# Kernel tuning notes

Measured on AMD Instinct MI355X. Metric: run time of the kernel, lower is better.

The kernel has to match this reference:

```python
import jax, jax.numpy as jnp
import numpy as np

B, S, I, H, L, A = 32768, 1, 128, 256, 2, 32


def setup_inputs() -> dict:
    key = jax.random.key(0)
    ks = jax.random.split(key, 16)
    s_in = 1.0 / np.sqrt(H)  # PyTorch GRU init scale
    def u(k, shape):
        return jax.random.uniform(k, shape, jnp.float32, -s_in, s_in)
    return {
        "x": jax.random.normal(ks[0], (B, S, I), jnp.float32),
        "h": jax.random.normal(ks[1], (L, B, H), jnp.float32),
        # layer 0 GRU params (gate order: r, z, n as in PyTorch)
        "w_ih0": u(ks[2], (3 * H, I)),
        "w_hh0": u(ks[3], (3 * H, H)),
        "b_ih0": u(ks[4], (3 * H,)),
        "b_hh0": u(ks[5], (3 * H,)),
        # layer 1 GRU params
        "w_ih1": u(ks[6], (3 * H, H)),
        "w_hh1": u(ks[7], (3 * H, H)),
        "b_ih1": u(ks[8], (3 * H,)),
        "b_hh1": u(ks[9], (3 * H,)),
        # heads
        "w_p": u(ks[10], (A, H)),
        "b_p": u(ks[11], (A,)),
        "w_v": u(ks[12], (1, H)),
        "b_v": u(ks[13], (1,)),
    }


def _gru_cell(x, h, w_ih, w_hh, b_ih, b_hh):
    # x: [B, in], h: [B, H]; PyTorch GRUCell math with gate order r,z,n
    gi = x @ w_ih.T + b_ih          # [B, 3H]
    gh = h @ w_hh.T + b_hh          # [B, 3H]
    i_r, i_z, i_n = jnp.split(gi, 3, axis=-1)
    h_r, h_z, h_n = jnp.split(gh, 3, axis=-1)
    r = jax.nn.sigmoid(i_r + h_r)
    z = jax.nn.sigmoid(i_z + h_z)
    n = jnp.tanh(i_n + r * h_n)
    return (1.0 - z) * n + z * h


def reference(x, h, w_ih0, w_hh0, b_ih0, b_hh0, w_ih1, w_hh1, b_ih1, b_hh1,
              w_p, b_p, w_v, b_v):
    xt = x[:, -1, :]  # seq len 1 -> single step
    h0 = _gru_cell(xt, h[0], w_ih0, w_hh0, b_ih0, b_hh0)
    h1 = _gru_cell(h0, h[1], w_ih1, w_hh1, b_ih1, b_hh1)
    logits = h1 @ w_p.T + b_p                 # [B, A]
    value = (h1 @ w_v.T + b_v)[:, 0]          # [B]
    h_new = jnp.stack([h0, h1], axis=0)       # [L, B, H]
    return logits, value, h_new
```

## Files before the change

### kernel.cpp

```cpp
#include <hip/hip_runtime.h>
#include <hip/hip_bf16.h>
#include <stdint.h>

#define NB 32768
#define ID 128
#define HD 256
#define AD 32
#define BM 32
#define MT 2
#define NTH 256
#define NBLK (NB / BM)

typedef unsigned int u32;
typedef unsigned short u16;
typedef __attribute__((ext_vector_type(8))) short bf16x8;
typedef __attribute__((ext_vector_type(4))) float f32x4;
typedef __attribute__((ext_vector_type(2))) u32 u32x2;

#define OFF_W0X 0
#define OFF_W0H 98304
#define OFF_W1X 294912
#define OFF_W1H 491520
#define OFF_WHD 688128
#define W_TOTAL 700416

__device__ __forceinline__ u16 f2bf(float f) {
    u32 u = __builtin_bit_cast(u32, f);
    return (u16)((u + 0x7FFFu + ((u >> 16) & 1u)) >> 16);
}
__device__ __forceinline__ float bf2f(u16 b) {
    return __builtin_bit_cast(float, (u32)b << 16);
}
__device__ __forceinline__ float sigf(float v) { return 1.0f / (1.0f + __expf(-v)); }
__device__ __forceinline__ float tanh_fast(float v) { return 1.0f - 2.0f / (1.0f + __expf(2.0f * v)); }

__global__ void prep_weights(const float* __restrict__ wih0, const float* __restrict__ whh0,
                             const float* __restrict__ wih1, const float* __restrict__ whh1,
                             const float* __restrict__ wp, const float* __restrict__ wv,
                             u16* __restrict__ wb) {
    int i = blockIdx.x * blockDim.x + threadIdx.x;
    if (i >= W_TOTAL) return;
    float v;
    if (i < OFF_W0H)      v = wih0[i];
    else if (i < OFF_W1X) v = whh0[i - OFF_W0H];
    else if (i < OFF_W1H) v = wih1[i - OFF_W1X];
    else if (i < OFF_WHD) v = whh1[i - OFF_W1H];
    else {
        int j = i - OFF_WHD;
        int r = j >> 8, k = j & 255;
        v = (r < AD) ? wp[j] : ((r == AD) ? wv[k] : 0.0f);
    }
    wb[i] = f2bf(v);
}

#define SWZ(row, kbyte, rowstride) ((((row) * (rowstride)) + (kbyte)) ^ (((row) & 7) << 4))

#define MFMA(a, b, c) __builtin_amdgcn_mfma_f32_16x16x32_bf16((a), (b), (c), 0, 0, 0)

template<int KXS>
__device__ __forceinline__ void stage_step(char* dst, const u16* __restrict__ Wx,
                                           const u16* __restrict__ Wh,
                                           int s, int cbase, int w, int lane) {
    const bool xside = s < KXS;
    const u16* W = xside ? Wx : Wh;
    const int KW = xside ? KXS * 32 : HD;
    const int ks = xside ? s : s - KXS;
#pragma unroll
    for (int i = 0; i < 3; ++i) {
        const int unit = w * 3 + i;
        const int ldsrow = unit * 16 + (lane >> 2);
        const int slot = lane & 3;
        const int g = ldsrow >> 6, colr = ldsrow & 63;
        const int kslot = slot ^ ((ldsrow >> 1) & 3);
        const u16* src = W + (size_t)(g * HD + cbase + colr) * KW + ks * 32 + kslot * 8;
        __builtin_amdgcn_global_load_lds(
            (const __attribute__((address_space(1))) void*)src,
            (__attribute__((address_space(3))) void*)(dst + unit * 1024),
            16, 0, 0);
    }
}

__device__ __forceinline__ bf16x8 read_wfrag(const char* buf, int g, int colw, int kg) {
    const int row = g * 64 + colw;
    const int slot = kg ^ ((row >> 1) & 3);
    return *(const bf16x8*)(buf + row * 64 + slot * 16);
}

template<int KXS>
__device__ __forceinline__ void gru_layer_v3(
    const char* __restrict__ Ax, const char* __restrict__ Ah,
    char* __restrict__ wb0, char* __restrict__ wb1,
    const u16* __restrict__ Wx, const u16* __restrict__ Wh,
    const float* __restrict__ bi, const float* __restrict__ bh,
    int lane, int w, u32 st[4][MT][2])
{
    constexpr int NS = KXS + 8;
    const int arow = lane & 15;
    const int kg = lane >> 4;
    const int colw = (w << 4) + arow;

#pragma unroll 1
    for (int c = 0; c < 4; ++c) {
        const int cbase = c * 64;
        const int col = cbase + colw;
        const float br  = bi[col] + bh[col];
        const float bz  = bi[HD + col] + bh[HD + col];
        const float bni = bi[2 * HD + col];
        const float bnh = bh[2 * HD + col];
        f32x4 accr[MT], accz[MT], accni[MT], accnh[MT];
#pragma unroll
        for (int m = 0; m < MT; ++m) {
            accr[m]  = f32x4{br, br, br, br};
            accz[m]  = f32x4{bz, bz, bz, bz};
            accni[m] = f32x4{bni, bni, bni, bni};
            accnh[m] = f32x4{bnh, bnh, bnh, bnh};
        }

        stage_step<KXS>(wb0, Wx, Wh, 0, cbase, w, lane);
        __syncthreads();

#pragma unroll
        for (int s = 0; s < NS; ++s) {
            char* cur = (s & 1) ? wb1 : wb0;
            char* nxt = (s & 1) ? wb0 : wb1;
            if (s + 1 < NS)
                stage_step<KXS>(nxt, Wx, Wh, s + 1, cbase, w, lane);
            bf16x8 w0 = read_wfrag(cur, 0, colw, kg);
            bf16x8 w1 = read_wfrag(cur, 1, colw, kg);
            bf16x8 w2 = read_wfrag(cur, 2, colw, kg);
            const bool xside = (s < KXS);
            const int kb2 = ((xside ? s : s - KXS) * 32 + kg * 8) * 2;
#pragma unroll
            for (int m = 0; m < MT; ++m) {
                const int row = m * 16 + arow;
                bf16x8 a = xside ? *(const bf16x8*)(Ax + SWZ(row, kb2, KXS * 64))
                                 : *(const bf16x8*)(Ah + SWZ(row, kb2, 512));
                accr[m] = MFMA(a, w0, accr[m]);
                accz[m] = MFMA(a, w1, accz[m]);
                if (xside) accni[m] = MFMA(a, w2, accni[m]);
                else       accnh[m] = MFMA(a, w2, accnh[m]);
            }
            __syncthreads();
        }

#pragma unroll
        for (int m = 0; m < MT; ++m) {
            const int rowg = m * 16 + ((lane >> 4) << 2);
#pragma unroll
            for (int pq = 0; pq < 2; ++pq) {
                u32 pk = 0;
#pragma unroll
                for (int q2 = 0; q2 < 2; ++q2) {
                    const int q = pq * 2 + q2;
                    float rg = sigf(accr[m][q]);
                    float zg = sigf(accz[m][q]);
                    float n  = tanh_fast(accni[m][q] + rg * accnh[m][q]);
                    float hp = bf2f(*(const u16*)(Ah + SWZ(rowg + q, col * 2, 512)));
                    float hv = (1.0f - zg) * n + zg * hp;
                    pk |= (u32)f2bf(hv) << (16 * q2);
                }
                st[c][m][pq] = pk;
            }
        }
    }
}

__device__ __forceinline__ void write_stash(char* __restrict__ R, u32 st[4][MT][2],
                                            int lane, int w) {
#pragma unroll
    for (int c = 0; c < 4; ++c)
#pragma unroll
        for (int m = 0; m < MT; ++m) {
            const int colb = (c * 64 + (w << 4) + (lane & 15)) * 2;
            const int rowg = m * 16 + ((lane >> 4) << 2);
            *(u16*)(R + SWZ(rowg + 0, colb, 512)) = (u16)(st[c][m][0]);
            *(u16*)(R + SWZ(rowg + 1, colb, 512)) = (u16)(st[c][m][0] >> 16);
            *(u16*)(R + SWZ(rowg + 2, colb, 512)) = (u16)(st[c][m][1]);
            *(u16*)(R + SWZ(rowg + 3, colb, 512)) = (u16)(st[c][m][1] >> 16);
        }
}

__device__ __forceinline__ void dump_h(const char* __restrict__ R,
                                       float* __restrict__ g, int row0, int t) {
#pragma unroll
    for (int it = 0; it < 8; ++it) {
        int i = t + it * NTH;
        int row = i >> 6, f4 = i & 63;
        u32x2 b = *(const u32x2*)(R + SWZ(row, f4 * 8, 512));
        f32x4 v;
        v[0] = __builtin_bit_cast(float, (b[0] & 0xFFFFu) << 16);
        v[1] = __builtin_bit_cast(float, b[0] & 0xFFFF0000u);
        v[2] = __builtin_bit_cast(float, (b[1] & 0xFFFFu) << 16);
        v[3] = __builtin_bit_cast(float, b[1] & 0xFFFF0000u);
        __builtin_nontemporal_store(v, (f32x4*)(g + (size_t)(row0 + row) * HD + f4 * 4));
    }
}

__global__ __launch_bounds__(NTH, 2) void gru_mfma(
    const float* __restrict__ x, const float* __restrict__ h,
    const float* __restrict__ bih0, const float* __restrict__ bhh0,
    const float* __restrict__ bih1, const float* __restrict__ bhh1,
    const float* __restrict__ bp, const float* __restrict__ bv,
    const u16* __restrict__ wb, float* __restrict__ out)
{
    __shared__ uint4 lds4[65536 / 16];
    char* lds = (char*)lds4;
    char* R1 = lds;
    char* R2 = lds + 8192;
    char* R3 = lds + 24576;
    char* WB0 = lds + 40960;
    char* WB1 = lds + 53248;

    const int t = threadIdx.x;
    const int lane = t & 63;
    const int w = t >> 6;
    const int row0 = blockIdx.x * BM;

    const u16* W0x = wb + OFF_W0X;
    const u16* W0h = wb + OFF_W0H;
    const u16* W1x = wb + OFF_W1X;
    const u16* W1h = wb + OFF_W1H;
    const u16* Whd = wb + OFF_WHD;

    float* out_logits = out;
    float* out_value  = out + (size_t)NB * AD;
    float* out_h0     = out_value + NB;
    float* out_h1     = out_h0 + (size_t)NB * HD;

    {
        const f32x4* xg = (const f32x4*)(x + (size_t)row0 * ID);
#pragma unroll
        for (int it = 0; it < 4; ++it) {
            int i = t + it * NTH;
            f32x4 v = __builtin_nontemporal_load(xg + i);
            int rowi = i >> 5;
            int kb = (i & 31) * 8;
            u32x2 b;
            b[0] = (u32)f2bf(v[0]) | ((u32)f2bf(v[1]) << 16);
            b[1] = (u32)f2bf(v[2]) | ((u32)f2bf(v[3]) << 16);
            *(u32x2*)(R1 + SWZ(rowi, kb, 256)) = b;
        }
        const f32x4* h0g = (const f32x4*)(h + (size_t)row0 * HD);
        const f32x4* h1g = (const f32x4*)(h + (size_t)NB * HD + (size_t)row0 * HD);
#pragma unroll
        for (int it = 0; it < 8; ++it) {
            int i = t + it * NTH;
            int rowi = i >> 6;
            int kb = (i & 63) * 8;
            f32x4 v0 = __builtin_nontemporal_load(h0g + i);
            u32x2 b0;
            b0[0] = (u32)f2bf(v0[0]) | ((u32)f2bf(v0[1]) << 16);
            b0[1] = (u32)f2bf(v0[2]) | ((u32)f2bf(v0[3]) << 16);
            *(u32x2*)(R2 + SWZ(rowi, kb, 512)) = b0;
            f32x4 v1 = __builtin_nontemporal_load(h1g + i);
            u32x2 b1;
            b1[0] = (u32)f2bf(v1[0]) | ((u32)f2bf(v1[1]) << 16);
            b1[1] = (u32)f2bf(v1[2]) | ((u32)f2bf(v1[3]) << 16);
            *(u32x2*)(R3 + SWZ(rowi, kb, 512)) = b1;
        }
    }
    __syncthreads();

    u32 st[4][MT][2];
    gru_layer_v3<4>(R1, R2, WB0, WB1, W0x, W0h, bih0, bhh0, lane, w, st);
    __syncthreads();
    write_stash(R2, st, lane, w);
    __syncthreads();
    dump_h(R2, out_h0, row0, t);

    gru_layer_v3<8>(R2, R3, WB0, WB1, W1x, W1h, bih1, bhh1, lane, w, st);
    __syncthreads();
    write_stash(R2, st, lane, w);
    __syncthreads();
    dump_h(R2, out_h1, row0, t);

    if (w < MT) {
        const int m = w;
        const int arow = lane & 15;
        const int krow = (lane >> 4) * 8;
        float b0 = bp[arow], b1 = bp[16 + arow], b2 = bv[0];
        f32x4 acc[3];
        acc[0] = f32x4{b0, b0, b0, b0};
        acc[1] = f32x4{b1, b1, b1, b1};
        acc[2] = f32x4{b2, b2, b2, b2};
#pragma unroll
        for (int ks = 0; ks < 8; ++ks) {
            const int kb = ks * 32 + krow;
            const int row = m * 16 + arow;
            bf16x8 a = *(const bf16x8*)(R2 + SWZ(row, kb * 2, 512));
#pragma unroll
            for (int f = 0; f < 3; ++f) {
                bf16x8 wf = *(const bf16x8*)(Whd + (size_t)(f * 16 + arow) * HD + kb);
                acc[f] = MFMA(a, wf, acc[f]);
            }
        }
        const int rowg = m * 16 + ((lane >> 4) << 2);
#pragma unroll
        for (int q = 0; q < 4; ++q) {
            __builtin_nontemporal_store(acc[0][q],
                &out_logits[(size_t)(row0 + rowg + q) * AD + arow]);
            __builtin_nontemporal_store(acc[1][q],
                &out_logits[(size_t)(row0 + rowg + q) * AD + 16 + arow]);
        }
        if (arow == 0) {
#pragma unroll
            for (int q = 0; q < 4; ++q)
                __builtin_nontemporal_store(acc[2][q], &out_value[row0 + rowg + q]);
        }
    }
}

extern "C" void kernel_launch(void* const* d_in, const int* in_sizes, int n_in,
                              void* d_out, int out_size, void* d_ws, size_t ws_size,
                              hipStream_t stream) {
    const float* x    = (const float*)d_in[0];
    const float* h    = (const float*)d_in[1];
    const float* wih0 = (const float*)d_in[2];
    const float* whh0 = (const float*)d_in[3];
    const float* bih0 = (const float*)d_in[4];
    const float* bhh0 = (const float*)d_in[5];
    const float* wih1 = (const float*)d_in[6];
    const float* whh1 = (const float*)d_in[7];
    const float* bih1 = (const float*)d_in[8];
    const float* bhh1 = (const float*)d_in[9];
    const float* wp   = (const float*)d_in[10];
    const float* bp   = (const float*)d_in[11];
    const float* wv   = (const float*)d_in[12];
    const float* bv   = (const float*)d_in[13];

    u16* wb = (u16*)d_ws;
    prep_weights<<<(W_TOTAL + 255) / 256, 256, 0, stream>>>(wih0, whh0, wih1, whh1, wp, wv, wb);
    gru_mfma<<<NBLK, NTH, 0, stream>>>(x, h, bih0, bhh0, bih1, bhh1, bp, bv, wb, (float*)d_out);
}
```

Measured before the change: 253.6 us.

## Triple-buffer per-wave weight staging and drop block barriers in GRU loop

Replaces the double-buffered weight staging with a three-slot ring and a two-step lookahead. The weight-loading assignment is remapped so each wave loads exactly the rows it later reads, which lets per-wave vmcnt waits replace the per-step __syncthreads. The four column chunks are merged into one fully unrolled step loop so prefetch continues across chunk boundaries, and biases are hoisted. The cost is a larger LDS footprint (about 76KB per block), which still has to fit two blocks per CU, plus a much longer unrolled body that can raise register pressure and instruction-cache load.

```diff
diff --git a/kernel.cpp b/kernel.cpp
--- a/kernel.cpp
+++ b/kernel.cpp
@@ -57,29 +57,6 @@
 
 #define MFMA(a, b, c) __builtin_amdgcn_mfma_f32_16x16x32_bf16((a), (b), (c), 0, 0, 0)
 
-template<int KXS>
-__device__ __forceinline__ void stage_step(char* dst, const u16* __restrict__ Wx,
-                                           const u16* __restrict__ Wh,
-                                           int s, int cbase, int w, int lane) {
-    const bool xside = s < KXS;
-    const u16* W = xside ? Wx : Wh;
-    const int KW = xside ? KXS * 32 : HD;
-    const int ks = xside ? s : s - KXS;
-#pragma unroll
-    for (int i = 0; i < 3; ++i) {
-        const int unit = w * 3 + i;
-        const int ldsrow = unit * 16 + (lane >> 2);
-        const int slot = lane & 3;
-        const int g = ldsrow >> 6, colr = ldsrow & 63;
-        const int kslot = slot ^ ((ldsrow >> 1) & 3);
-        const u16* src = W + (size_t)(g * HD + cbase + colr) * KW + ks * 32 + kslot * 8;
-        __builtin_amdgcn_global_load_lds(
-            (const __attribute__((address_space(1))) void*)src,
-            (__attribute__((address_space(3))) void*)(dst + unit * 1024),
-            16, 0, 0);
-    }
-}
-
 __device__ __forceinline__ bf16x8 read_wfrag(const char* buf, int g, int colw, int kg) {
     const int row = g * 64 + colw;
     const int slot = kg ^ ((row >> 1) & 3);
@@ -87,79 +64,114 @@
 }
 
 template<int KXS>
-__device__ __forceinline__ void gru_layer_v3(
+__device__ __forceinline__ void gru_layer_v4(
     const char* __restrict__ Ax, const char* __restrict__ Ah,
-    char* __restrict__ wb0, char* __restrict__ wb1,
+    char* __restrict__ wbuf,
     const u16* __restrict__ Wx, const u16* __restrict__ Wh,
     const float* __restrict__ bi, const float* __restrict__ bh,
     int lane, int w, u32 st[4][MT][2])
 {
-    constexpr int NS = KXS + 8;
+    constexpr int NSL = KXS + 8;
+    constexpr int NS = 4 * NSL;
     const int arow = lane & 15;
     const int kg = lane >> 4;
     const int colw = (w << 4) + arow;
 
-#pragma unroll 1
+    float brv[4], bzv[4], bniv[4], bnhv[4];
+#pragma unroll
     for (int c = 0; c < 4; ++c) {
-        const int cbase = c * 64;
-        const int col = cbase + colw;
-        const float br  = bi[col] + bh[col];
-        const float bz  = bi[HD + col] + bh[HD + col];
-        const float bni = bi[2 * HD + col];
-        const float bnh = bh[2 * HD + col];
-        f32x4 accr[MT], accz[MT], accni[MT], accnh[MT];
+        const int col = c * 64 + colw;
+        brv[c]  = bi[col] + bh[col];
+        bzv[c]  = bi[HD + col] + bh[HD + col];
+        bniv[c] = bi[2 * HD + col];
+        bnhv[c] = bh[2 * HD + col];
+    }
+    asm volatile("s_waitcnt vmcnt(0)" ::: "memory");
+
+    auto stage = [&](int sg2) {
+        const int c2 = sg2 / NSL, ss2 = sg2 - c2 * NSL;
+        const bool xs = ss2 < KXS;
+        const u16* W = xs ? Wx : Wh;
+        const int KW = xs ? KXS * 32 : HD;
+        const int ks = xs ? ss2 : ss2 - KXS;
+        char* dst = wbuf + (sg2 % 3) * 12288;
+#pragma unroll
+        for (int i = 0; i < 3; ++i) {
+            const int unit = i * 4 + w;
+            const int ldsrow = unit * 16 + (lane >> 2);
+            const int colr = ldsrow & 63;
+            const int kslot = (lane & 3) ^ ((ldsrow >> 1) & 3);
+            const u16* src = W + (size_t)(i * HD + c2 * 64 + colr) * KW + ks * 32 + kslot * 8;
+            __builtin_amdgcn_global_load_lds(
+                (const __attribute__((address_space(1))) void*)src,
+                (__attribute__((address_space(3))) void*)(dst + unit * 1024),
+                16, 0, 0);
+        }
+    };
+
+    f32x4 accr[MT], accz[MT], accni[MT], accnh[MT];
+
+    stage(0);
+    stage(1);
+#pragma unroll
+    for (int sg = 0; sg < NS; ++sg) {
+        const int c = sg / NSL, ss = sg - c * NSL;
+        if (ss == 0) {
+#pragma unroll
+            for (int m = 0; m < MT; ++m) {
+                accr[m]  = f32x4{brv[c], brv[c], brv[c], brv[c]};
+                accz[m]  = f32x4{bzv[c], bzv[c], bzv[c], bzv[c]};
+                accni[m] = f32x4{bniv[c], bniv[c], bniv[c], bniv[c]};
+                accnh[m] = f32x4{bnhv[c], bnhv[c], bnhv[c], bnhv[c]};
+            }
+        }
+        if (sg + 2 < NS) {
+            stage(sg + 2);
+            asm volatile("s_waitcnt vmcnt(6)" ::: "memory");
+        } else if (sg + 1 < NS) {
+            asm volatile("s_waitcnt vmcnt(3)" ::: "memory");
+        } else {
+            asm volatile("s_waitcnt vmcnt(0)" ::: "memory");
+        }
+        __builtin_amdgcn_sched_barrier(0);
+
+        const char* cur = wbuf + (sg % 3) * 12288;
+        bf16x8 w0 = read_wfrag(cur, 0, colw, kg);
+        bf16x8 w1 = read_wfrag(cur, 1, colw, kg);
+        bf16x8 w2 = read_wfrag(cur, 2, colw, kg);
+        const bool xside = ss < KXS;
+        const int kb2 = ((xside ? ss : ss - KXS) * 32 + kg * 8) * 2;
 #pragma unroll
         for (int m = 0; m < MT; ++m) {
-            accr[m]  = f32x4{br, br, br, br};
-            accz[m]  = f32x4{bz, bz, bz, bz};
-            accni[m] = f32x4{bni, bni, bni, bni};
-            accnh[m] = f32x4{bnh, bnh, bnh, bnh};
-        }
-
-        stage_step<KXS>(wb0, Wx, Wh, 0, cbase, w, lane);
-        __syncthreads();
-
-#pragma unroll
-        for (int s = 0; s < NS; ++s) {
-            char* cur = (s & 1) ? wb1 : wb0;
-            char* nxt = (s & 1) ? wb0 : wb1;
-            if (s + 1 < NS)
-                stage_step<KXS>(nxt, Wx, Wh, s + 1, cbase, w, lane);
-            bf16x8 w0 = read_wfrag(cur, 0, colw, kg);
-            bf16x8 w1 = read_wfrag(cur, 1, colw, kg);
-            bf16x8 w2 = read_wfrag(cur, 2, colw, kg);
-            const bool xside = (s < KXS);
-            const int kb2 = ((xside ? s : s - KXS) * 32 + kg * 8) * 2;
+            const int row = m * 16 + arow;
+            bf16x8 a = xside ? *(const bf16x8*)(Ax + SWZ(row, kb2, KXS * 64))
+                             : *(const bf16x8*)(Ah + SWZ(row, kb2, 512));
+            accr[m] = MFMA(a, w0, accr[m]);
+            accz[m] = MFMA(a, w1, accz[m]);
+            if (xside) accni[m] = MFMA(a, w2, accni[m]);
+            else       accnh[m] = MFMA(a, w2, accnh[m]);
+        }
+
+        if (ss == NSL - 1) {
+            const int col = c * 64 + colw;
 #pragma unroll
             for (int m = 0; m < MT; ++m) {
-                const int row = m * 16 + arow;
-                bf16x8 a = xside ? *(const bf16x8*)(Ax + SWZ(row, kb2, KXS * 64))
-                                 : *(const bf16x8*)(Ah + SWZ(row, kb2, 512));
-                accr[m] = MFMA(a, w0, accr[m]);
-                accz[m] = MFMA(a, w1, accz[m]);
-                if (xside) accni[m] = MFMA(a, w2, accni[m]);
-                else       accnh[m] = MFMA(a, w2, accnh[m]);
-            }
-            __syncthreads();
-        }
-
-#pragma unroll
-        for (int m = 0; m < MT; ++m) {
-            const int rowg = m * 16 + ((lane >> 4) << 2);
-#pragma unroll
-            for (int pq = 0; pq < 2; ++pq) {
-                u32 pk = 0;
-#pragma unroll
-                for (int q2 = 0; q2 < 2; ++q2) {
-                    const int q = pq * 2 + q2;
-                    float rg = sigf(accr[m][q]);
-                    float zg = sigf(accz[m][q]);
-                    float n  = tanh_fast(accni[m][q] + rg * accnh[m][q]);
-                    float hp = bf2f(*(const u16*)(Ah + SWZ(rowg + q, col * 2, 512)));
-                    float hv = (1.0f - zg) * n + zg * hp;
-                    pk |= (u32)f2bf(hv) << (16 * q2);
+                const int rowg = m * 16 + ((lane >> 4) << 2);
+#pragma unroll
+                for (int pq = 0; pq < 2; ++pq) {
+                    u32 pk = 0;
+#pragma unroll
+                    for (int q2 = 0; q2 < 2; ++q2) {
+                        const int q = pq * 2 + q2;
+                        float rg = sigf(accr[m][q]);
+                        float zg = sigf(accz[m][q]);
+                        float n  = tanh_fast(accni[m][q] + rg * accnh[m][q]);
+                        float hp = bf2f(*(const u16*)(Ah + SWZ(rowg + q, col * 2, 512)));
+                        float hv = (1.0f - zg) * n + zg * hp;
+                        pk |= (u32)f2bf(hv) << (16 * q2);
+                    }
+                    st[c][m][pq] = pk;
                 }
-                st[c][m][pq] = pk;
             }
         }
     }
@@ -203,13 +215,12 @@
     const float* __restrict__ bp, const float* __restrict__ bv,
     const u16* __restrict__ wb, float* __restrict__ out)
 {
-    __shared__ uint4 lds4[65536 / 16];
+    __shared__ uint4 lds4[77824 / 16];
     char* lds = (char*)lds4;
     char* R1 = lds;
     char* R2 = lds + 8192;
     char* R3 = lds + 24576;
-    char* WB0 = lds + 40960;
-    char* WB1 = lds + 53248;
+    char* WBUF = lds + 40960;
 
     const int t = threadIdx.x;
     const int lane = t & 63;
@@ -262,13 +273,13 @@
     __syncthreads();
 
     u32 st[4][MT][2];
-    gru_layer_v3<4>(R1, R2, WB0, WB1, W0x, W0h, bih0, bhh0, lane, w, st);
+    gru_layer_v4<4>(R1, R2, WBUF, W0x, W0h, bih0, bhh0, lane, w, st);
     __syncthreads();
     write_stash(R2, st, lane, w);
     __syncthreads();
     dump_h(R2, out_h0, row0, t);
 
-    gru_layer_v3<8>(R2, R3, WB0, WB1, W1x, W1h, bih1, bhh1, lane, w, st);
+    gru_layer_v4<8>(R2, R3, WBUF, W1x, W1h, bih1, bhh1, lane, w, st);
     __syncthreads();
     write_stash(R2, st, lane, w);
     __syncthreads();
```

Result: slower. 293.9 us (+15.9%).
